# Performance work log

Hardware: AMD Instinct MI355X
Metric: run time of the kernel (lower is better)

Reference implementation:

```python
import jax, jax.numpy as jnp
import numpy as np

D, M, B = 4096, 1024, 64

def build_tile_idx(D, b):
    T = D // (2 * b)
    d4 = D // 4
    hb = b // 2
    t = np.arange(T)
    # horizontal tiles: view x as (D/4, 4); rows t*hb..(t+1)*hb, cols 0..3
    rows = t[:, None, None] * hb + np.arange(hb)[None, :, None]          # (T, hb, 1)
    horiz = (rows * 4 + np.arange(4)[None, None, :]).reshape(T, -1)      # (T, 2b)
    # vertical tiles: view x as (4, D/4); rows 0..3, cols t*hb..(t+1)*hb
    cols = t[:, None, None] * hb + np.arange(hb)[None, None, :]          # (T, 1, hb)
    vert = (np.arange(4)[None, :, None] * d4 + cols).reshape(T, -1)      # (T, 2b)
    return np.concatenate([horiz, vert], axis=0)                          # (G=2T, 2b)

def setup_inputs() -> dict:
    key = jax.random.key(0)
    k1, k2 = jax.random.split(key)
    N = 2048
    T = D // (2 * B)
    G = 2 * T
    e = M // G                     # experts per group
    tile_size = 2 * B
    x_flat = jax.random.normal(k1, (N, D), dtype=jnp.float32)
    V = jax.random.normal(k2, (G, e, tile_size, B), dtype=jnp.float32)
    tile_idx = jnp.asarray(build_tile_idx(D, B), dtype=jnp.int32)
    return {"x_flat": x_flat, "V": V, "tile_idx": tile_idx}

def reference(x_flat, V, tile_idx):
    # UnitColNorm(dim=2): normalize V columns along the tile_size axis
    Vn = V / jnp.linalg.norm(V, axis=2, keepdims=True)
    # gather tiles: (N, G, tile_size)
    x_tiles = x_flat[:, tile_idx]
    # grouped batched matmul: (N,G,t) x (G,e,t,b) -> (N,G,e,b)
    h = jnp.einsum('ngt,getb->ngeb', x_tiles, Vn)
    N = x_flat.shape[0]
    return h.reshape(N, M, B)
```

## Files before the change

### kernel.cpp

```cpp
#include <hip/hip_runtime.h>
#include <hip/hip_bf16.h>

typedef short s16x8 __attribute__((ext_vector_type(8)));
typedef float f32x16 __attribute__((ext_vector_type(16)));

#define D_DIM 4096
#define OUT_STRIDE 65536

__device__ __forceinline__ unsigned int f2bf(float f) {
    unsigned int u = __float_as_uint(f);
    u += 0x7FFFu + ((u >> 16) & 1u);
    return u >> 16;
}
__device__ __forceinline__ unsigned int pk2(float a, float b) {
    return f2bf(a) | (f2bf(b) << 16);
}

__global__ __launch_bounds__(256) void vnorm_kernel(const float* __restrict__ V,
                                                    unsigned short* __restrict__ Bn) {
    const int blk = blockIdx.x;
    const int tid = threadIdx.x;
    const float* Vt = V + (size_t)blk * 8192;
    __shared__ float tile[8192];
    __shared__ float part[256];
    __shared__ float rnorm[64];

    for (int i = tid; i < 2048; i += 256)
        ((float4*)tile)[i] = ((const float4*)Vt)[i];
    __syncthreads();

    {
        int b = tid & 63, q = tid >> 6;
        float s = 0.f;
        for (int t = q; t < 128; t += 4) { float v = tile[t * 64 + b]; s += v * v; }
        part[tid] = s;
    }
    __syncthreads();
    if (tid < 64) {
        float tot = part[tid] + part[tid + 64] + part[tid + 128] + part[tid + 192];
        rnorm[tid] = rsqrtf(tot);
    }
    __syncthreads();

    unsigned short* rowbase = Bn + (size_t)blk * 64 * 128;
    for (int iter = 0; iter < 4; ++iter) {
        int idx = iter * 256 + tid;
        int b = idx >> 4, k8 = idx & 15;
        float rn = rnorm[b];
        unsigned int w[4];
        int tb = k8 * 8;
        #pragma unroll
        for (int j = 0; j < 4; ++j) {
            float v0 = tile[(tb + 2 * j) * 64 + b] * rn;
            float v1 = tile[(tb + 2 * j + 1) * 64 + b] * rn;
            w[j] = pk2(v0, v1);
        }
        uint4* dst = (uint4*)(rowbase + b * 128) + k8;
        *dst = make_uint4(w[0], w[1], w[2], w[3]);
    }
}

__global__ __launch_bounds__(1024, 4) void gemm_kernel(const float* __restrict__ x,
                                                       const unsigned short* __restrict__ Bn,
                                                       float* __restrict__ out) {
    const int s = blockIdx.x;
    const int g = blockIdx.y;
    const int tid = threadIdx.x;
    const int lane = tid & 63, wv = tid >> 6;
    const int jl = lane & 31, hi = lane >> 5;
    const int m_base = s * 512;

    __shared__ __align__(16) unsigned short Alds[2][16384];

    s16x8 bfrag[2][8];
    {
        const char* Bbase = (const char*)(Bn + (size_t)g * 131072);
        #pragma unroll
        for (int nf = 0; nf < 2; ++nf) {
            const char* rb = Bbase + (wv * 64 + nf * 32 + jl) * 256 + hi * 16;
            #pragma unroll
            for (int ks = 0; ks < 8; ++ks)
                bfrag[nf][ks] = *(const s16x8*)(rb + ks * 32);
        }
    }

    const int swz = (jl & 7) << 4;

    #define STAGE(MC, BUF)                                                        \
        {                                                                         \
            _Pragma("unroll")                                                     \
            for (int p = 0; p < 2; ++p) {                                         \
                int c = tid + p * 1024;                                           \
                int r = c >> 4, kc = c & 15;                                      \
                int k0 = kc * 8;                                                  \
                int idx = (g < 32) ? (g * 128 + k0)                               \
                                   : ((k0 >> 5) * 1024 + (g - 32) * 32 + (k0 & 31)); \
                const float* xp = x + (size_t)(m_base + (MC) * 128 + r) * D_DIM + idx; \
                float4 v0 = *(const float4*)xp;                                   \
                float4 v1 = *(const float4*)(xp + 4);                             \
                uint4 w = make_uint4(pk2(v0.x, v0.y), pk2(v0.z, v0.w),            \
                                     pk2(v1.x, v1.y), pk2(v1.z, v1.w));           \
                *(uint4*)((char*)Alds[BUF] + r * 256 + ((kc * 16) ^ ((r & 7) << 4))) = w; \
            }                                                                     \
        }

    STAGE(0, 0);

    #pragma unroll
    for (int mc = 0; mc < 4; ++mc) {
        asm volatile("s_waitcnt lgkmcnt(0)" ::: "memory");
        __builtin_amdgcn_s_barrier();
        asm volatile("" ::: "memory");

        if (mc < 3) STAGE(mc + 1, (mc + 1) & 1);

        const char* Acur = (const char*)Alds[mc & 1];
        const int m0 = m_base + mc * 128;
        #pragma unroll
        for (int rs = 0; rs < 4; ++rs) {
            const char* Ab = Acur + (rs * 32 + jl) * 256;
            f32x16 acc0 = {0.f}, acc1 = {0.f};
            #pragma unroll
            for (int ks = 0; ks < 8; ++ks) {
                s16x8 a = *(const s16x8*)(Ab + ((ks * 32 + hi * 16) ^ swz));
                acc0 = __builtin_amdgcn_mfma_f32_32x32x16_bf16(a, bfrag[0][ks], acc0, 0, 0, 0);
                acc1 = __builtin_amdgcn_mfma_f32_32x32x16_bf16(a, bfrag[1][ks], acc1, 0, 0, 0);
            }
            float* obase = out + (size_t)(m0 + rs * 32 + 4 * hi) * OUT_STRIDE
                         + g * 1024 + wv * 64 + jl;
            #pragma unroll
            for (int reg = 0; reg < 16; ++reg) {
                int row = (reg & 3) + 8 * (reg >> 2);
                float* p = obase + (size_t)row * OUT_STRIDE;
                __builtin_nontemporal_store(acc0[reg], p);
                __builtin_nontemporal_store(acc1[reg], p + 32);
            }
        }
    }
    #undef STAGE
}

extern "C" void kernel_launch(void* const* d_in, const int* in_sizes, int n_in,
                              void* d_out, int out_size, void* d_ws, size_t ws_size,
                              hipStream_t stream) {
    const float* x = (const float*)d_in[0];
    const float* V = (const float*)d_in[1];
    float* out = (float*)d_out;
    unsigned short* Bn = (unsigned short*)d_ws;

    const int N = in_sizes[0] / D_DIM;
    const int nsplit = N / 512;

    vnorm_kernel<<<1024, 256, 0, stream>>>(V, Bn);
    gemm_kernel<<<dim3(nsplit, 64), 1024, 0, stream>>>(x, Bn, out);
}
```

Before: 140.9 us.

## Fuse V column normalization into GEMM by scaling outputs with reciprocal norms

Removes the separate vnorm kernel and its bf16 workspace round-trip. Each wave now loads raw fp32 V directly, packs it to bf16 fragments, computes column sums of squares with a cross-half shuffle, and multiplies the accumulators by the reciprocal norm before storing. This saves a kernel launch and an intermediate write and read. In exchange, V is read redundantly by each of the N/512 row splits, the fp32 loads are strided and uncoalesced, and rounding differs slightly because normalization now happens after the matmul.

```diff
diff --git a/kernel.cpp b/kernel.cpp
--- a/kernel.cpp
+++ b/kernel.cpp
@@ -16,52 +16,8 @@
     return f2bf(a) | (f2bf(b) << 16);
 }
 
-__global__ __launch_bounds__(256) void vnorm_kernel(const float* __restrict__ V,
-                                                    unsigned short* __restrict__ Bn) {
-    const int blk = blockIdx.x;
-    const int tid = threadIdx.x;
-    const float* Vt = V + (size_t)blk * 8192;
-    __shared__ float tile[8192];
-    __shared__ float part[256];
-    __shared__ float rnorm[64];
-
-    for (int i = tid; i < 2048; i += 256)
-        ((float4*)tile)[i] = ((const float4*)Vt)[i];
-    __syncthreads();
-
-    {
-        int b = tid & 63, q = tid >> 6;
-        float s = 0.f;
-        for (int t = q; t < 128; t += 4) { float v = tile[t * 64 + b]; s += v * v; }
-        part[tid] = s;
-    }
-    __syncthreads();
-    if (tid < 64) {
-        float tot = part[tid] + part[tid + 64] + part[tid + 128] + part[tid + 192];
-        rnorm[tid] = rsqrtf(tot);
-    }
-    __syncthreads();
-
-    unsigned short* rowbase = Bn + (size_t)blk * 64 * 128;
-    for (int iter = 0; iter < 4; ++iter) {
-        int idx = iter * 256 + tid;
-        int b = idx >> 4, k8 = idx & 15;
-        float rn = rnorm[b];
-        unsigned int w[4];
-        int tb = k8 * 8;
-        #pragma unroll
-        for (int j = 0; j < 4; ++j) {
-            float v0 = tile[(tb + 2 * j) * 64 + b] * rn;
-            float v1 = tile[(tb + 2 * j + 1) * 64 + b] * rn;
-            w[j] = pk2(v0, v1);
-        }
-        uint4* dst = (uint4*)(rowbase + b * 128) + k8;
-        *dst = make_uint4(w[0], w[1], w[2], w[3]);
-    }
-}
-
 __global__ __launch_bounds__(1024, 4) void gemm_kernel(const float* __restrict__ x,
-                                                       const unsigned short* __restrict__ Bn,
+                                                       const float* __restrict__ V,
                                                        float* __restrict__ out) {
     const int s = blockIdx.x;
     const int g = blockIdx.y;
@@ -73,15 +29,35 @@
     __shared__ __align__(16) unsigned short Alds[2][16384];
 
     s16x8 bfrag[2][8];
+    float rn0, rn1;
     {
-        const char* Bbase = (const char*)(Bn + (size_t)g * 131072);
+        const float* Vp = V + (size_t)(g * 16 + wv) * 8192;
+        float s0 = 0.f, s1 = 0.f;
         #pragma unroll
-        for (int nf = 0; nf < 2; ++nf) {
-            const char* rb = Bbase + (wv * 64 + nf * 32 + jl) * 256 + hi * 16;
+        for (int ks = 0; ks < 8; ++ks) {
+            unsigned int w0[4], w1[4];
             #pragma unroll
-            for (int ks = 0; ks < 8; ++ks)
-                bfrag[nf][ks] = *(const s16x8*)(rb + ks * 32);
+            for (int i = 0; i < 4; ++i) {
+                int t = ks * 16 + hi * 8 + 2 * i;
+                float a0 = Vp[t * 64 + jl];
+                float b0 = Vp[(t + 1) * 64 + jl];
+                float a1 = Vp[t * 64 + 32 + jl];
+                float b1 = Vp[(t + 1) * 64 + 32 + jl];
+                s0 += a0 * a0 + b0 * b0;
+                s1 += a1 * a1 + b1 * b1;
+                w0[i] = pk2(a0, b0);
+                w1[i] = pk2(a1, b1);
+            }
+            union { uint4 u; s16x8 v; } p0, p1;
+            p0.u = make_uint4(w0[0], w0[1], w0[2], w0[3]);
+            p1.u = make_uint4(w1[0], w1[1], w1[2], w1[3]);
+            bfrag[0][ks] = p0.v;
+            bfrag[1][ks] = p1.v;
         }
+        s0 += __shfl_xor(s0, 32, 64);
+        s1 += __shfl_xor(s1, 32, 64);
+        rn0 = rsqrtf(s0);
+        rn1 = rsqrtf(s1);
     }
 
     const int swz = (jl & 7) << 4;
@@ -132,8 +108,8 @@
             for (int reg = 0; reg < 16; ++reg) {
                 int row = (reg & 3) + 8 * (reg >> 2);
                 float* p = obase + (size_t)row * OUT_STRIDE;
-                __builtin_nontemporal_store(acc0[reg], p);
-                __builtin_nontemporal_store(acc1[reg], p + 32);
+                __builtin_nontemporal_store(acc0[reg] * rn0, p);
+                __builtin_nontemporal_store(acc1[reg] * rn1, p + 32);
             }
         }
     }
@@ -146,11 +122,9 @@
     const float* x = (const float*)d_in[0];
     const float* V = (const float*)d_in[1];
     float* out = (float*)d_out;
-    unsigned short* Bn = (unsigned short*)d_ws;
 
     const int N = in_sizes[0] / D_DIM;
     const int nsplit = N / 512;
 
-    vnorm_kernel<<<1024, 256, 0, stream>>>(V, Bn);
-    gemm_kernel<<<dim3(nsplit, 64), 1024, 0, stream>>>(x, Bn, out);
+    gemm_kernel<<<dim3(nsplit, 64), 1024, 0, stream>>>(x, V, out);
 }
```

After: 141.1 us. No clear change (+0.1%).
